# Kernel optimization log

Measured on AMD Instinct MI355X. Metric: run time of the kernel, lower is better.

Reference implementation:

```python
import jax, jax.numpy as jnp
import numpy as np

B, L, S, STATIC = 32, 512, 37, 8
D, DI, N, K, DTR, NL, V = 768, 1536, 16, 4, 48, 4, 32


def _rmsnorm(h, w, eps=1e-5):
    var = jnp.mean(h * h, axis=-1, keepdims=True)
    return h * jax.lax.rsqrt(var + eps) * w


def _layernorm(h, w, b, eps=1e-5):
    mu = jnp.mean(h, axis=-1, keepdims=True)
    var = jnp.mean((h - mu) ** 2, axis=-1, keepdims=True)
    return (h - mu) * jax.lax.rsqrt(var + eps) * w + b


def _selective_scan(u, dt, A, Bm, Cm):
    # u, dt: [B,L,Di]; A: [Di,N]; Bm, Cm: [B,L,N]
    def step(h, inp):
        u_t, dt_t, B_t, C_t = inp              # [B,Di],[B,Di],[B,N],[B,N]
        dA = jnp.exp(dt_t[..., None] * A)      # [B,Di,N]
        h = dA * h + (dt_t * u_t)[..., None] * B_t[:, None, :]
        y = jnp.einsum('bdn,bn->bd', h, C_t)
        return h, y
    h0 = jnp.zeros((u.shape[0], DI, N), u.dtype)
    xs = (u.transpose(1, 0, 2), dt.transpose(1, 0, 2),
          Bm.transpose(1, 0, 2), Cm.transpose(1, 0, 2))
    _, ys = jax.lax.scan(step, h0, xs)
    return ys.transpose(1, 0, 2)  # [B,L,Di]


def setup_inputs() -> dict:
    key = jax.random.key(0)
    ks = jax.random.split(key, 24)
    s = 0.02
    inp = {
        'x': jax.random.normal(ks[0], (B, L, S), jnp.float32),
        'static': jax.random.normal(ks[1], (B, STATIC), jnp.float32),
        'time': jax.random.uniform(ks[2], (B, L), jnp.float32),
        'sensor_mask': jax.random.randint(ks[3], (B, L, S), 0, 2, jnp.int32),
        'labels': jax.random.randint(ks[4], (B, L), 0, V, jnp.int64),
        # CEHR embedding params
        'emb_w': jax.random.normal(ks[5], (D, 2 * S), jnp.float32) * s,
        'emb_b': jnp.zeros((D,), jnp.float32),
        'static_w': jax.random.normal(ks[6], (D, STATIC), jnp.float32) * s,
        'static_b': jnp.zeros((D,), jnp.float32),
        'ln_w': jnp.ones((D,), jnp.float32),
        'ln_b': jnp.zeros((D,), jnp.float32),
        # Mamba layers (stacked)
        'norm_w': jnp.ones((NL, D), jnp.float32),
        'in_proj_w': jax.random.normal(ks[7], (NL, 2 * DI, D), jnp.float32) * s,
        'conv_w': jax.random.normal(ks[8], (NL, DI, K), jnp.float32) * s,
        'conv_b': jnp.zeros((NL, DI), jnp.float32),
        'x_proj_w': jax.random.normal(ks[9], (NL, DTR + 2 * N, DI), jnp.float32) * s,
        'dt_proj_w': jax.random.normal(ks[10], (NL, DI, DTR), jnp.float32) * s,
        'dt_proj_b': jnp.full((NL, DI), -4.6, jnp.float32),  # softplus^-1(~0.01)
        'A_log': jnp.broadcast_to(jnp.log(jnp.arange(1, N + 1, dtype=jnp.float32)), (NL, DI, N)).copy(),
        'D_param': jnp.ones((NL, DI), jnp.float32),
        'out_proj_w': jax.random.normal(ks[11], (NL, D, DI), jnp.float32) * s,
        'norm_f_w': jnp.ones((D,), jnp.float32),
        'lm_head_w': jax.random.normal(ks[12], (V, D), jnp.float32) * s,
    }
    return inp


def reference(x, static, time, sensor_mask, labels, emb_w, emb_b, static_w,
              static_b, ln_w, ln_b, norm_w, in_proj_w, conv_w, conv_b,
              x_proj_w, dt_proj_w, dt_proj_b, A_log, D_param, out_proj_w,
              norm_f_w, lm_head_w):
    # ---- CEHR embedding: concat(values, mask) -> D, plus static broadcast ----
    feats = jnp.concatenate([x, sensor_mask.astype(x.dtype)], axis=-1)  # [B,L,2S]
    h = jnp.einsum('blf,df->bld', feats, emb_w) + emb_b
    h = h + (static @ static_w.T + static_b)[:, None, :]
    h = _layernorm(h, ln_w, ln_b)  # [B,L,D]

    # ---- Mamba backbone ----
    for l in range(NL):
        resid = h
        hn = _rmsnorm(h, norm_w[l])
        xz = jnp.einsum('bld,ed->ble', hn, in_proj_w[l])  # [B,L,2*Di]
        xb, z = jnp.split(xz, 2, axis=-1)
        # causal depthwise conv1d, kernel K
        xp = jnp.pad(xb, ((0, 0), (K - 1, 0), (0, 0)))
        xc = sum(conv_w[l][:, k] * xp[:, k:k + L, :] for k in range(K)) + conv_b[l]
        xc = jax.nn.silu(xc)
        proj = jnp.einsum('bld,ed->ble', xc, x_proj_w[l])  # [B,L,DTR+2N]
        dt_r = proj[..., :DTR]
        Bm = proj[..., DTR:DTR + N]
        Cm = proj[..., DTR + N:]
        dt = jax.nn.softplus(jnp.einsum('blr,dr->bld', dt_r, dt_proj_w[l]) + dt_proj_b[l])
        A = -jnp.exp(A_log[l])  # [Di,N]
        y = _selective_scan(xc, dt, A, Bm, Cm) + D_param[l] * xc
        y = y * jax.nn.silu(z)
        h = resid + jnp.einsum('ble,de->bld', y, out_proj_w[l])

    h = _rmsnorm(h, norm_f_w)
    logits = jnp.einsum('bld,vd->blv', h, lm_head_w)  # [B,L,V]
    return logits
```

## Files before the change

### kernel.cpp

```cpp
#include <hip/hip_runtime.h>
#include <math.h>

#define B_ 32
#define L_ 512
#define S_ 37
#define STATIC_ 8
#define D_ 768
#define DI_ 1536
#define N_ 16
#define DTR_ 48
#define NL_ 4
#define V_ 32
#define ROWS_ (B_*L_)
#define CB_ 8
#define CROWS_ (CB_*L_)
#define NCH_ (B_/CB_)
#define KE_ 96
#define TCH_ 64
#define NCHT_ (L_/TCH_)
#define TP4_ 68
#define KS_ 4
#define KSL_ (DI_/KS_)

typedef __bf16 bf16;
typedef __bf16 bf16x8 __attribute__((ext_vector_type(8)));
typedef __bf16 bf16x4 __attribute__((ext_vector_type(4)));
typedef __bf16 bf16x2 __attribute__((ext_vector_type(2)));
typedef float f32x4 __attribute__((ext_vector_type(4)));

typedef __attribute__((address_space(3))) void lds_void;
typedef __attribute__((address_space(1))) const void gmem_void;

__device__ __forceinline__ void gld16(const void* g, void* l) {
    __builtin_amdgcn_global_load_lds((gmem_void*)g, (lds_void*)l, 16, 0, 0);
}

__device__ __forceinline__ float silu_(float x) { return x / (1.f + __expf(-x)); }
__device__ __forceinline__ float softplus_(float x) {
    return fmaxf(x, 0.f) + __logf(1.f + __expf(-fabsf(x)));
}
__device__ __forceinline__ unsigned pack_bf2_(float a, float b) {
    bf16x2 v{(bf16)a, (bf16)b};
    return __builtin_bit_cast(unsigned, v);
}
template<int CTRL>
__device__ __forceinline__ float dpp_add_(float p) {
    int vi = __builtin_amdgcn_update_dpp(0, __builtin_bit_cast(int, p),
                                         CTRL, 0xF, 0xF, true);
    return p + __builtin_bit_cast(float, vi);
}

template<int MODE>
__global__ __launch_bounds__(256) void gemm_mfma(
    const bf16* __restrict__ A, const bf16* __restrict__ W,
    const float* __restrict__ addsrc, void* __restrict__ Cv,
    int Nstore, int K, int ntn,
    const float* __restrict__ dt_bias, unsigned* __restrict__ swg,
    float* __restrict__ pbuf, const bf16* __restrict__ uref)
{
    __shared__ bf16 As[128 * 32];
    __shared__ bf16 Bs[128 * 32];
    const int tid = threadIdx.x;

    int m0, n0, kbeg, kend;
    if (MODE == 4) {
        m0 = blockIdx.y * 128; n0 = 0;
        kbeg = blockIdx.x * KSL_; kend = kbeg + KSL_;
    } else {
        int bid = blockIdx.x;
        int xcd = bid & 7, slot = bid >> 3;
        int Mtiles = gridDim.x / ntn;
        int mband = Mtiles >> 3;
        int m_tile = xcd * mband + slot / ntn;
        int n_tile = slot % ntn;
        m0 = m_tile * 128; n0 = n_tile * 128;
        kbeg = 0; kend = K;
    }

    f32x4 acc[4][4];
    #pragma unroll
    for (int i = 0; i < 4; i++)
        #pragma unroll
        for (int j = 0; j < 4; j++)
            acc[i][j] = f32x4{0.f, 0.f, 0.f, 0.f};

    const int srow = tid >> 2, spart = tid & 3;
    const bf16* ag = A + (size_t)(m0 + srow) * K + spart * 8;
    const bf16* wg = W + (size_t)(n0 + srow) * K + spart * 8;
    char* lA = (char*)As + tid * 16;
    char* lB = (char*)Bs + tid * 16;

    const int lane = tid & 63, wv = tid >> 6;
    const int wr = wv >> 1, wc = wv & 1;
    const int colL = lane & 15, quad = lane >> 4;
    const bf16* aRd = As + (wr * 64 + colL) * 32 + quad * 8;
    const bf16* bRd = Bs + (wc * 64 + colL) * 32 + quad * 8;

    for (int kt = kbeg; kt < kend; kt += 32) {
        gld16(ag + kt, lA);
        gld16(ag + kt + (size_t)64 * K, lA + 4096);
        gld16(wg + kt, lB);
        gld16(wg + kt + (size_t)64 * K, lB + 4096);
        __syncthreads();
        bf16x8 fa[4], fb[4];
        #pragma unroll
        for (int i = 0; i < 4; i++) fa[i] = *(const bf16x8*)(aRd + i * 16 * 32);
        #pragma unroll
        for (int j = 0; j < 4; j++) fb[j] = *(const bf16x8*)(bRd + j * 16 * 32);
        #pragma unroll
        for (int i = 0; i < 4; i++)
            #pragma unroll
            for (int j = 0; j < 4; j++)
                acc[i][j] = __builtin_amdgcn_mfma_f32_16x16x32_bf16(fa[i], fb[j], acc[i][j], 0, 0, 0);
        __syncthreads();
    }

    float* Cf = (float*)Cv;
    bf16*  Cb = (bf16*)Cv;
    #pragma unroll
    for (int i = 0; i < 4; i++) {
        #pragma unroll
        for (int j = 0; j < 4; j++) {
            int n = n0 + wc * 64 + j * 16 + colL;
            #pragma unroll
            for (int r = 0; r < 4; r++) {
                int m = m0 + wr * 64 + i * 16 + quad * 4 + r;
                float v = acc[i][j][r];
                if (MODE == 2) {
                    float dtv = softplus_(v + dt_bias[n]);
                    float u = (float)uref[(size_t)m * DI_ + n];
                    swg[(size_t)m * DI_ + n] = pack_bf2_(dtv * u, dtv);
                } else if (MODE == 4) {
                    if (n < 96)
                        pbuf[((size_t)blockIdx.x * CROWS_ + m) * 96 + n] = v;
                } else if (n < Nstore) {
                    if (addsrc) v += addsrc[(size_t)m * Nstore + n];
                    if (MODE == 1) Cb[(size_t)m * Nstore + n] = (bf16)v;
                    else           Cf[(size_t)m * Nstore + n] = v;
                }
            }
        }
    }
}

template<int MODE>
__global__ __launch_bounds__(512, 2) void gemm256(
    const bf16* __restrict__ A, const bf16* __restrict__ W,
    const float* __restrict__ addsrc, void* __restrict__ Cv,
    int Nstore, int K, int ntn)
{
    __shared__ bf16 lds[65536];
    const int tid = threadIdx.x;

    const int bid = blockIdx.x;
    const int qx = gridDim.x >> 3;
    const int wgid = (bid & 7) * qx + (bid >> 3);
    const int m0 = (wgid / ntn) * 256;
    const int n0 = (wgid % ntn) * 256;

    const int r0 = tid >> 3;
    const int scol = ((tid & 7) * 8) ^ ((r0 & 7) << 3);
    const size_t sK = (size_t)K;
    const bf16* aSrc = A + (size_t)(m0 + r0) * sK + scol;
    const bf16* bSrc = W + (size_t)(n0 + r0) * sK + scol;
    char* ldst = (char*)lds + tid * 16;

#define STAGE_A(h, t) { const bf16* s_ = aSrc + (size_t)(h) * 128 * sK + (t) * 64;   \
    char* d_ = ldst + ((t) & 1) * 65536 + (h) * 16384;                               \
    gld16(s_, d_); gld16(s_ + 64 * sK, d_ + 8192); }
#define STAGE_B(h, t) { const bf16* s_ = bSrc + (size_t)(h) * 128 * sK + (t) * 64;   \
    char* d_ = ldst + ((t) & 1) * 65536 + 32768 + (h) * 16384;                       \
    gld16(s_, d_); gld16(s_ + 64 * sK, d_ + 8192); }

    const int lane = tid & 63, w = tid >> 6;
    const int wr = w >> 2, wc = w & 3;
    const int colL = lane & 15, quad = lane >> 4;
    const int sx = (colL & 7) << 3;
    const int c0 = (quad * 8) ^ sx;
    const int c1 = c0 ^ 32;
    const bf16* aRd0 = lds + wr * 8192 + colL * 64 + c0;
    const bf16* aRd1 = lds + wr * 8192 + colL * 64 + c1;
    const bf16* bRd0 = lds + 16384 + (wc >> 1) * 8192 + ((wc & 1) * 64 + colL) * 64 + c0;
    const bf16* bRd1 = lds + 16384 + (wc >> 1) * 8192 + ((wc & 1) * 64 + colL) * 64 + c1;

    f32x4 acc[8][4];
    #pragma unroll
    for (int i = 0; i < 8; i++)
        #pragma unroll
        for (int j = 0; j < 4; j++)
            acc[i][j] = f32x4{0.f, 0.f, 0.f, 0.f};
    bf16x8 aF[4][2], bF[4][2];

#define RD_A(buf, mp) { _Pragma("unroll") for (int i = 0; i < 4; i++) {              \
    aF[i][0] = *(const bf16x8*)(aRd0 + (buf) * 32768 + (mp) * 4096 + i * 1024);      \
    aF[i][1] = *(const bf16x8*)(aRd1 + (buf) * 32768 + (mp) * 4096 + i * 1024); } }
#define RD_B01(buf) { _Pragma("unroll") for (int j = 0; j < 2; j++) {                \
    bF[j][0] = *(const bf16x8*)(bRd0 + (buf) * 32768 + j * 1024);                    \
    bF[j][1] = *(const bf16x8*)(bRd1 + (buf) * 32768 + j * 1024); } }
#define RD_B23(buf) { _Pragma("unroll") for (int j = 0; j < 2; j++) {                \
    bF[2 + j][0] = *(const bf16x8*)(bRd0 + (buf) * 32768 + (2 + j) * 1024);          \
    bF[2 + j][1] = *(const bf16x8*)(bRd1 + (buf) * 32768 + (2 + j) * 1024); } }
#define MM(mp, np) { _Pragma("unroll") for (int i = 0; i < 4; i++)                   \
    _Pragma("unroll") for (int j = 0; j < 2; j++) {                                  \
    acc[(mp)*4+i][(np)*2+j] = __builtin_amdgcn_mfma_f32_16x16x32_bf16(               \
        aF[i][0], bF[(np)*2+j][0], acc[(mp)*4+i][(np)*2+j], 0, 0, 0);                \
    acc[(mp)*4+i][(np)*2+j] = __builtin_amdgcn_mfma_f32_16x16x32_bf16(               \
        aF[i][1], bF[(np)*2+j][1], acc[(mp)*4+i][(np)*2+j], 0, 0, 0); } }
#define MID_SYNC  __builtin_amdgcn_s_barrier();                                      \
    asm volatile("s_waitcnt lgkmcnt(0)" ::: "memory");                               \
    __builtin_amdgcn_sched_barrier(0);                                               \
    __builtin_amdgcn_s_setprio(1);
#define END_PHASE __builtin_amdgcn_s_setprio(0); __builtin_amdgcn_s_barrier();

    const int NT = K >> 6;
    const int NI = NT >> 1;

    STAGE_B(0, 0); STAGE_B(1, 0); STAGE_A(0, 0); STAGE_A(1, 0);
    STAGE_B(0, 1); STAGE_B(1, 1);
    asm volatile("s_waitcnt vmcnt(4)" ::: "memory");
    __builtin_amdgcn_s_barrier();

    for (int it = 0; it < NI; ++it) {
        const int t0 = 2 * it, t1 = t0 + 1;
        const bool nlast = (it + 1 < NI);
        RD_A(0, 0); RD_B01(0);
        STAGE_A(0, t1);
        MID_SYNC; MM(0, 0); END_PHASE;
        RD_B23(0);
        STAGE_A(1, t1);
        MID_SYNC; MM(0, 1); END_PHASE;
        RD_A(0, 1);
        if (nlast) STAGE_B(0, t0 + 2);
        MID_SYNC; MM(1, 0); END_PHASE;
        if (nlast) STAGE_B(1, t0 + 2);
        MID_SYNC; MM(1, 1);
        __builtin_amdgcn_s_setprio(0);
        if (nlast) { asm volatile("s_waitcnt vmcnt(4)" ::: "memory"); }
        else       { asm volatile("s_waitcnt vmcnt(0)" ::: "memory"); }
        __builtin_amdgcn_s_barrier();
        RD_A(1, 0); RD_B01(1);
        if (nlast) STAGE_A(0, t0 + 2);
        MID_SYNC; MM(0, 0); END_PHASE;
        RD_B23(1);
        if (nlast) STAGE_A(1, t0 + 2);
        MID_SYNC; MM(0, 1); END_PHASE;
        RD_A(1, 1);
        if (nlast) STAGE_B(0, t1 + 2);
        MID_SYNC; MM(1, 0); END_PHASE;
        if (nlast) STAGE_B(1, t1 + 2);
        MID_SYNC; MM(1, 1);
        __builtin_amdgcn_s_setprio(0);
        if (nlast) { asm volatile("s_waitcnt vmcnt(4)" ::: "memory"); }
        __builtin_amdgcn_s_barrier();
    }

    float* Cf = (float*)Cv;
    bf16*  Cb = (bf16*)Cv;
    #pragma unroll
    for (int f = 0; f < 8; f++) {
        #pragma unroll
        for (int j = 0; j < 4; j++) {
            int n = n0 + wc * 64 + j * 16 + colL;
            #pragma unroll
            for (int r = 0; r < 4; r++) {
                int m = m0 + wr * 128 + f * 16 + quad * 4 + r;
                float v = acc[f][j][r];
                if (MODE == 0) {
                    v += addsrc[(size_t)m * Nstore + n];
                    Cf[(size_t)m * Nstore + n] = v;
                } else {
                    Cb[(size_t)m * Nstore + n] = (bf16)v;
                }
            }
        }
    }
#undef STAGE_A
#undef STAGE_B
#undef RD_A
#undef RD_B01
#undef RD_B23
#undef MM
#undef MID_SYNC
#undef END_PHASE
}

__global__ __launch_bounds__(256) void xpost_kernel(const float* __restrict__ pbuf,
                                                    bf16* __restrict__ dtr,
                                                    bf16* __restrict__ bcb) {
    int idx = blockIdx.x * 256 + threadIdx.x;
    int m = idx / 96, j = idx % 96;
    float s = pbuf[idx];
    #pragma unroll
    for (int k = 1; k < KS_; k++) s += pbuf[(size_t)k * CROWS_ * 96 + idx];
    if (j < 64) {
        dtr[(size_t)m * 64 + j] = (bf16)s;
    } else {
        int jj = j - 64;
        int n = jj & 15, hi = jj >> 4;
        bcb[(size_t)m * 32 + 2 * n + hi] = (bf16)s;
    }
}

__global__ __launch_bounds__(256) void cast_f2b_kernel(const float* __restrict__ s,
                                                       bf16* __restrict__ d) {
    size_t i = (size_t)blockIdx.x * 256 + threadIdx.x;
    d[i] = (bf16)s[i];
}

__global__ __launch_bounds__(256) void pad_lm_kernel(const float* __restrict__ s, bf16* __restrict__ d) {
    int i = blockIdx.x * 256 + threadIdx.x;
    int row = i / D_;
    d[i] = (row < V_) ? (bf16)s[i] : (bf16)0.f;
}

__global__ __launch_bounds__(256) void pad_embw_kernel(const float* __restrict__ s, bf16* __restrict__ d) {
    int i = blockIdx.x * 256 + threadIdx.x;
    int row = i / KE_, col = i % KE_;
    d[i] = (col < 2 * S_) ? (bf16)s[row * 2 * S_ + col] : (bf16)0.f;
}

__global__ __launch_bounds__(256) void feats_kernel(const float* __restrict__ x,
                                                    const int* __restrict__ mask,
                                                    bf16* __restrict__ d) {
    size_t i = (size_t)blockIdx.x * 256 + threadIdx.x;
    size_t row = i / KE_;
    int col = (int)(i % KE_);
    float v = 0.f;
    if (col < S_) v = x[row * S_ + col];
    else if (col < 2 * S_) v = (float)mask[row * S_ + (col - S_)];
    d[i] = (bf16)v;
}

__global__ __launch_bounds__(256) void xpw_pad_kernel(const float* __restrict__ xpw,
                                                      bf16* __restrict__ d) {
    int l = blockIdx.y;
    int idx = blockIdx.x * 256 + threadIdx.x;
    int row = idx / DI_, col = idx % DI_;
    float v = 0.f;
    if (row < DTR_) v = xpw[((size_t)l * (DTR_ + 2 * N_) + row) * DI_ + col];
    else if (row >= 64 && row < 96) v = xpw[((size_t)l * (DTR_ + 2 * N_) + row - 16) * DI_ + col];
    d[(size_t)l * 128 * DI_ + idx] = (bf16)v;
}

__global__ __launch_bounds__(256) void dtw_pad_kernel(const float* __restrict__ dtw,
                                                      bf16* __restrict__ d) {
    int l = blockIdx.y;
    int idx = blockIdx.x * 256 + threadIdx.x;
    int row = idx / 64, c = idx % 64;
    float v = (c < DTR_) ? dtw[((size_t)l * DI_ + row) * DTR_ + c] : 0.f;
    d[(size_t)l * DI_ * 64 + idx] = (bf16)v;
}

__global__ __launch_bounds__(256) void sstat_kernel(const float* __restrict__ stat,
                                                    const float* __restrict__ static_w,
                                                    const float* __restrict__ static_b,
                                                    const float* __restrict__ emb_b,
                                                    float* __restrict__ sstat) {
    int i = blockIdx.x * 256 + threadIdx.x;
    int d = i % D_, b = i / D_;
    float acc = emb_b[d] + static_b[d];
    const float* sw = static_w + (size_t)d * STATIC_;
    const float* sv = stat + (size_t)b * STATIC_;
    #pragma unroll
    for (int s = 0; s < STATIC_; s++) acc += sv[s] * sw[s];
    sstat[i] = acc;
}

__device__ __forceinline__ void block_reduce2_(float& a, float& b, float* sbuf) {
    #pragma unroll
    for (int off = 32; off > 0; off >>= 1) {
        a += __shfl_down(a, off, 64);
        b += __shfl_down(b, off, 64);
    }
    int lane = threadIdx.x & 63, wid = threadIdx.x >> 6;
    if (lane == 0) { sbuf[wid] = a; sbuf[4 + wid] = b; }
    __syncthreads();
    a = sbuf[0] + sbuf[1] + sbuf[2] + sbuf[3];
    b = sbuf[4] + sbuf[5] + sbuf[6] + sbuf[7];
}

__global__ __launch_bounds__(256) void ln_embed_kernel(const float* __restrict__ h_pre,
                                                       const float* __restrict__ sstat,
                                                       const float* __restrict__ ln_w,
                                                       const float* __restrict__ ln_b,
                                                       float* __restrict__ h) {
    int row = blockIdx.x, b = row / L_, tid = threadIdx.x;
    __shared__ float sbuf[8];
    float v[3], sum = 0.f, sq = 0.f;
    #pragma unroll
    for (int j = 0; j < 3; j++) {
        int d = tid + 256 * j;
        v[j] = h_pre[(size_t)row * D_ + d] + sstat[b * D_ + d];
        sum += v[j]; sq += v[j] * v[j];
    }
    block_reduce2_(sum, sq, sbuf);
    float mu = sum * (1.f / D_);
    float rstd = rsqrtf(sq * (1.f / D_) - mu * mu + 1e-5f);
    #pragma unroll
    for (int j = 0; j < 3; j++) {
        int d = tid + 256 * j;
        h[(size_t)row * D_ + d] = (v[j] - mu) * rstd * ln_w[d] + ln_b[d];
    }
}

__global__ __launch_bounds__(256) void rmsnorm_bf_kernel(const float* __restrict__ h,
                                                         const float* __restrict__ w,
                                                         bf16* __restrict__ out) {
    int row = blockIdx.x, tid = threadIdx.x;
    __shared__ float sbuf[8];
    float v[3], ss = 0.f, dummy = 0.f;
    #pragma unroll
    for (int j = 0; j < 3; j++) {
        v[j] = h[(size_t)row * D_ + tid + 256 * j];
        ss += v[j] * v[j];
    }
    block_reduce2_(ss, dummy, sbuf);
    float rstd = rsqrtf(ss * (1.f / D_) + 1e-5f);
    #pragma unroll
    for (int j = 0; j < 3; j++) {
        int d = tid + 256 * j;
        out[(size_t)row * D_ + d] = (bf16)(v[j] * rstd * w[d]);
    }
}

__global__ __launch_bounds__(256) void conv_silu_kernel(const bf16* __restrict__ xzb,
                                                        const float* __restrict__ cw,
                                                        const float* __restrict__ cb,
                                                        const float* __restrict__ Dp,
                                                        bf16* __restrict__ xcb,
                                                        unsigned* __restrict__ gag) {
    size_t idx = (size_t)blockIdx.x * 256 + threadIdx.x;
    int d4 = (int)(idx % (DI_ / 4));
    size_t row = idx / (DI_ / 4);
    int t = (int)(row % L_);
    int d = d4 * 4;
    const uint2* xz64 = (const uint2*)xzb;
    size_t base = row * 768 + d4;
    uint2 z2{0u, 0u};
    uint2 p0  = xz64[base];
    uint2 pm1 = (t >= 1) ? xz64[base - 768]     : z2;
    uint2 pm2 = (t >= 2) ? xz64[base - 2 * 768] : z2;
    uint2 pm3 = (t >= 3) ? xz64[base - 3 * 768] : z2;
    uint2 pz  = xz64[base + 384];

    bf16x4 a0 = __builtin_bit_cast(bf16x4, p0);
    bf16x4 a1 = __builtin_bit_cast(bf16x4, pm1);
    bf16x4 a2 = __builtin_bit_cast(bf16x4, pm2);
    bf16x4 a3 = __builtin_bit_cast(bf16x4, pm3);
    bf16x4 az = __builtin_bit_cast(bf16x4, pz);

    float cbl[4], Dl[4];
    *(float4*)cbl = ((const float4*)cb)[d4];
    *(float4*)Dl  = ((const float4*)Dp)[d4];

    float u[4];
    unsigned gv[4];
    #pragma unroll
    for (int c = 0; c < 4; c++) {
        float4 wc = ((const float4*)cw)[d + c];
        float acc = cbl[c] + wc.x * (float)a3[c] + wc.y * (float)a2[c]
                           + wc.z * (float)a1[c] + wc.w * (float)a0[c];
        u[c] = silu_(acc);
        float gz = silu_((float)az[c]);
        gv[c] = pack_bf2_(Dl[c] * u[c] * gz, gz);
    }
    ((uint2*)xcb)[row * (DI_ / 4) + d4] = uint2{pack_bf2_(u[0], u[1]), pack_bf2_(u[2], u[3])};
    *(uint4*)(gag + row * DI_ + d) = uint4{gv[0], gv[1], gv[2], gv[3]};
}

__global__ __launch_bounds__(256) void scan_lds_kernel(const unsigned* __restrict__ bcp,
                                                       const unsigned* __restrict__ swg,
                                                       const unsigned* __restrict__ gag,
                                                       const float* __restrict__ A_log,
                                                       bf16* __restrict__ yb) {
    __shared__ unsigned lsw[2][16][TP4_];
    __shared__ unsigned lga[2][16][TP4_];
    __shared__ unsigned lbc[2][16][TP4_];
    const int tid = threadIdx.x;
    const int n = tid & 15, dl = tid >> 4;
    const int d = blockIdx.x * 16 + dl;
    const int b = blockIdx.y;
    const float AvL = -__expf(A_log[(size_t)d * N_ + n]) * 1.44269504f;
    const size_t seqbase = (size_t)b * L_;
    const int d0 = blockIdx.x * 16;

    unsigned swr[4], gar[4], bcr[4];

    #define GLOAD(c)                                                        \
        {                                                                   \
            size_t rb = seqbase + (size_t)(c) * TCH_;                       \
            _Pragma("unroll")                                               \
            for (int i = 0; i < 4; i++) {                                   \
                size_t g = rb + i * 16 + dl;                                \
                swr[i] = swg[g * DI_ + d0 + n];                             \
                gar[i] = gag[g * DI_ + d0 + n];                             \
                bcr[i] = bcp[g * 16 + n];                                   \
            }                                                               \
        }
    #define DSWRITE(p)                                                      \
        {                                                                   \
            _Pragma("unroll")                                               \
            for (int i = 0; i < 4; i++) {                                   \
                int t = i * 16 + dl;                                        \
                lsw[p][n][t] = swr[i];                                      \
                lga[p][n][t] = gar[i];                                      \
                lbc[p][n][t] = bcr[i];                                      \
            }                                                               \
        }

    GLOAD(0);
    DSWRITE(0);
    __syncthreads();
    GLOAD(1);

    float h = 0.f;
    for (int c = 0; c < NCHT_; c++) {
        int p = c & 1;
        bf16* py = yb + (seqbase + (size_t)c * TCH_) * DI_ + d;
        #pragma unroll 4
        for (int t0 = 0; t0 < TCH_; t0 += 4) {
            uint4 s4 = *(const uint4*)&lsw[p][dl][t0];
            uint4 b4 = *(const uint4*)&lbc[p][n][t0];
            uint4 g4{0u, 0u, 0u, 0u};
            if (n == 0) g4 = *(const uint4*)&lga[p][dl][t0];
            unsigned ss[4] = {s4.x, s4.y, s4.z, s4.w};
            unsigned bb[4] = {b4.x, b4.y, b4.z, b4.w};
            unsigned gg[4] = {g4.x, g4.y, g4.z, g4.w};
            #pragma unroll
            for (int u = 0; u < 4; u++) {
                bf16x2 dv = __builtin_bit_cast(bf16x2, ss[u]);
                bf16x2 bcv = __builtin_bit_cast(bf16x2, bb[u]);
                float du = (float)dv.x, dtv = (float)dv.y;
                float dA = __builtin_amdgcn_exp2f(dtv * AvL);
                h = dA * h + du * (float)bcv.x;
                float pq = h * (float)bcv.y;
                pq = dpp_add_<0xB1>(pq);
                pq = dpp_add_<0x4E>(pq);
                pq = dpp_add_<0x124>(pq);
                pq = dpp_add_<0x128>(pq);
                if (n == 0) {
                    bf16x2 og = __builtin_bit_cast(bf16x2, gg[u]);
                    py[(size_t)(t0 + u) * DI_] = (bf16)(pq * (float)og.y + (float)og.x);
                }
            }
        }
        if (c + 1 < NCHT_) {
            DSWRITE(p ^ 1);
            __syncthreads();
            if (c + 2 < NCHT_) GLOAD(c + 2);
        }
    }
    #undef GLOAD
    #undef DSWRITE
}

extern "C" void kernel_launch(void* const* d_in, const int* in_sizes, int n_in,
                              void* d_out, int out_size, void* d_ws, size_t ws_size,
                              hipStream_t stream) {
    const float* x        = (const float*)d_in[0];
    const float* stat     = (const float*)d_in[1];
    const int*   mask     = (const int*)d_in[3];
    const float* emb_w    = (const float*)d_in[5];
    const float* emb_b    = (const float*)d_in[6];
    const float* static_w = (const float*)d_in[7];
    const float* static_b = (const float*)d_in[8];
    const float* ln_w     = (const float*)d_in[9];
    const float* ln_b     = (const float*)d_in[10];
    const float* norm_w   = (const float*)d_in[11];
    const float* in_proj_w  = (const float*)d_in[12];
    const float* conv_w   = (const float*)d_in[13];
    const float* conv_b   = (const float*)d_in[14];
    const float* x_proj_w = (const float*)d_in[15];
    const float* dt_proj_w= (const float*)d_in[16];
    const float* dt_proj_b= (const float*)d_in[17];
    const float* A_log    = (const float*)d_in[18];
    const float* D_param  = (const float*)d_in[19];
    const float* out_proj_w = (const float*)d_in[20];
    const float* norm_f_w = (const float*)d_in[21];
    const float* lm_head_w= (const float*)d_in[22];
    float* out = (float*)d_out;

    char* p = (char*)d_ws;
    float*    h      = (float*)p;         p += (size_t)ROWS_ * D_ * 4;
    bf16*     hn_bf  = (bf16*)p;          p += (size_t)CROWS_ * D_ * 2;
    char*     xz_region = p;
    bf16*     xz_bf  = (bf16*)p;          p += (size_t)CROWS_ * 2 * DI_ * 2;
    bf16*     xc_bf  = (bf16*)p;          p += (size_t)CROWS_ * DI_ * 2;
    unsigned* sw_g   = (unsigned*)p;      p += (size_t)CROWS_ * DI_ * 4;
    unsigned* gate_g = (unsigned*)p;      p += (size_t)CROWS_ * DI_ * 4;
    bf16*     bc16   = (bf16*)p;          p += (size_t)CROWS_ * 32 * 2;
    bf16*     dtr_bf = (bf16*)p;          p += (size_t)CROWS_ * 64 * 2;
    float*    pbuf   = (float*)p;         p += (size_t)KS_ * CROWS_ * 96 * 4;
    bf16*     y_bf   = (bf16*)p;          p += (size_t)ROWS_ * DI_ * 2;
    bf16*     inw_l  = (bf16*)p;          p += (size_t)2 * DI_ * D_ * 2;
    bf16*     outw_l = (bf16*)p;          p += (size_t)D_ * DI_ * 2;
    bf16*     xpwp_bf= (bf16*)p;          p += (size_t)NL_ * 128 * DI_ * 2;
    bf16*     dtwp_bf= (bf16*)p;          p += (size_t)NL_ * DI_ * 64 * 2;
    bf16*     lmw_bf = (bf16*)p;          p += (size_t)128 * D_ * 2;
    bf16*     embw_bf= (bf16*)p;          p += (size_t)D_ * KE_ * 2;
    bf16*     feats  = (bf16*)p;          p += (size_t)ROWS_ * KE_ * 2;
    float*    sstat  = (float*)p;         p += (size_t)B_ * D_ * 4;
    float*    h_pre  = (float*)xz_region;
    bf16*     hn_full= (bf16*)sw_g;

    pad_lm_kernel<<<(128 * D_) / 256, 256, 0, stream>>>(lm_head_w, lmw_bf);
    pad_embw_kernel<<<(D_ * KE_) / 256, 256, 0, stream>>>(emb_w, embw_bf);
    feats_kernel<<<(ROWS_ * KE_) / 256, 256, 0, stream>>>(x, mask, feats);
    dim3 gxp((128 * DI_) / 256, NL_);
    xpw_pad_kernel<<<gxp, 256, 0, stream>>>(x_proj_w, xpwp_bf);
    dim3 gdt((DI_ * 64) / 256, NL_);
    dtw_pad_kernel<<<gdt, 256, 0, stream>>>(dt_proj_w, dtwp_bf);
    sstat_kernel<<<(B_ * D_) / 256, 256, 0, stream>>>(stat, static_w, static_b, emb_b, sstat);

    gemm_mfma<0><<<(D_ / 128) * (ROWS_ / 128), 256, 0, stream>>>(
        feats, embw_bf, nullptr, h_pre, D_, KE_, D_ / 128,
        nullptr, nullptr, nullptr, nullptr);
    ln_embed_kernel<<<ROWS_, 256, 0, stream>>>(h_pre, sstat, ln_w, ln_b, h);

    for (int l = 0; l < NL_; l++) {
        cast_f2b_kernel<<<(2 * DI_ * D_) / 256, 256, 0, stream>>>(
            in_proj_w + (size_t)l * 2 * DI_ * D_, inw_l);
        cast_f2b_kernel<<<(D_ * DI_) / 256, 256, 0, stream>>>(
            out_proj_w + (size_t)l * D_ * DI_, outw_l);

        for (int c = 0; c < NCH_; c++) {
            float* hc = h + (size_t)c * CROWS_ * D_;

            rmsnorm_bf_kernel<<<CROWS_, 256, 0, stream>>>(hc, norm_w + (size_t)l * D_, hn_bf);

            gemm256<1><<<(CROWS_ / 256) * (2 * DI_ / 256), 512, 0, stream>>>(
                hn_bf, inw_l, nullptr, xz_bf, 2 * DI_, D_, 2 * DI_ / 256);

            conv_silu_kernel<<<(CROWS_ * DI_ / 4) / 256, 256, 0, stream>>>(
                xz_bf, conv_w + (size_t)l * DI_ * 4, conv_b + (size_t)l * DI_,
                D_param + (size_t)l * DI_, xc_bf, gate_g);

            dim3 g2a(KS_, CROWS_ / 128);
            gemm_mfma<4><<<g2a, 256, 0, stream>>>(xc_bf, xpwp_bf + (size_t)l * 128 * DI_,
                                                  nullptr, nullptr, 0, DI_, 1,
                                                  nullptr, nullptr, pbuf, nullptr);
            xpost_kernel<<<(CROWS_ * 96) / 256, 256, 0, stream>>>(pbuf, dtr_bf, bc16);

            gemm_mfma<2><<<(DI_ / 128) * (CROWS_ / 128), 256, 0, stream>>>(
                dtr_bf, dtwp_bf + (size_t)l * DI_ * 64, nullptr, nullptr, 0, 64, DI_ / 128,
                dt_proj_b + (size_t)l * DI_, sw_g, nullptr, xc_bf);

            dim3 gs(DI_ / 16, CB_);
            scan_lds_kernel<<<gs, 256, 0, stream>>>((const unsigned*)bc16, sw_g, gate_g,
                                                    A_log + (size_t)l * DI_ * N_,
                                                    y_bf + (size_t)c * CROWS_ * DI_);
        }

        gemm256<0><<<(ROWS_ / 256) * (D_ / 256), 512, 0, stream>>>(
            y_bf, outw_l, h, h, D_, DI_, D_ / 256);
    }

    rmsnorm_bf_kernel<<<ROWS_, 256, 0, stream>>>(h, norm_f_w, hn_full);
    gemm_mfma<0><<<ROWS_ / 128, 256, 0, stream>>>(
        hn_full, lmw_bf, nullptr, out, V_, D_, 1,
        nullptr, nullptr, nullptr, nullptr);
}
```

Measured before the change: 2.740 ms.

## Restructure selective scan: fp32 swizzled B/C tiles, async LDS loads, batched output writes

xpost now writes B and C as fp32 into a per-chunk, XOR-swizzled 8KB tile layout. The scan kernel pulls these tiles straight into LDS with global_load_lds and double-buffers them. The scan kernel also stores dt/u pre-converted to float2 in LDS, which removes per-step bf16 conversions. The output is collected across 16 timesteps so that each lane writes one y value, replacing writes made only by lane n==0. This reduces ALU and store divergence in the scan inner loop, at the cost of doubling the B/C buffer size and using more LDS.

Measured after the change: 2.403 ms. 1.14x faster.

```diff
diff --git a/kernel.cpp b/kernel.cpp
--- a/kernel.cpp
+++ b/kernel.cpp
@@ -18,9 +18,10 @@
 #define KE_ 96
 #define TCH_ 64
 #define NCHT_ (L_/TCH_)
-#define TP4_ 68
 #define KS_ 4
 #define KSL_ (DI_/KS_)
+#define TPW_ 66
+#define TPO_ 68
 
 typedef __bf16 bf16;
 typedef __bf16 bf16x8 __attribute__((ext_vector_type(8)));
@@ -286,7 +287,7 @@
 
 __global__ __launch_bounds__(256) void xpost_kernel(const float* __restrict__ pbuf,
                                                     bf16* __restrict__ dtr,
-                                                    bf16* __restrict__ bcb) {
+                                                    float* __restrict__ bcf) {
     int idx = blockIdx.x * 256 + threadIdx.x;
     int m = idx / 96, j = idx % 96;
     float s = pbuf[idx];
@@ -297,7 +298,10 @@
     } else {
         int jj = j - 64;
         int n = jj & 15, hi = jj >> 4;
-        bcb[(size_t)m * 32 + 2 * n + hi] = (bf16)s;
+        int bb = m >> 9, t = m & 511;
+        int ct = t >> 6, tl = t & 63;
+        int byo = (n * 512 + tl * 8 + hi * 4) ^ ((n & 7) << 4);
+        *(float*)((char*)bcf + (size_t)(bb * 8 + ct) * 8192 + byo) = s;
     }
 }
 
@@ -468,89 +472,86 @@
     *(uint4*)(gag + row * DI_ + d) = uint4{gv[0], gv[1], gv[2], gv[3]};
 }
 
-__global__ __launch_bounds__(256) void scan_lds_kernel(const unsigned* __restrict__ bcp,
+__global__ __launch_bounds__(256) void scan_lds_kernel(const float* __restrict__ bcf,
                                                        const unsigned* __restrict__ swg,
                                                        const unsigned* __restrict__ gag,
                                                        const float* __restrict__ A_log,
                                                        bf16* __restrict__ yb) {
-    __shared__ unsigned lsw[2][16][TP4_];
-    __shared__ unsigned lga[2][16][TP4_];
-    __shared__ unsigned lbc[2][16][TP4_];
+    __shared__ float2   lsw2[2][16][TPW_];
+    __shared__ char     lbcf[2][8192];
+    __shared__ unsigned logds[2][16][TPO_];
     const int tid = threadIdx.x;
     const int n = tid & 15, dl = tid >> 4;
-    const int d = blockIdx.x * 16 + dl;
+    const int d0 = blockIdx.x * 16;
+    const int d = d0 + dl;
     const int b = blockIdx.y;
     const float AvL = -__expf(A_log[(size_t)d * N_ + n]) * 1.44269504f;
     const size_t seqbase = (size_t)b * L_;
-    const int d0 = blockIdx.x * 16;
-
-    unsigned swr[4], gar[4], bcr[4];
-
-    #define GLOAD(c)                                                        \
-        {                                                                   \
-            size_t rb = seqbase + (size_t)(c) * TCH_;                       \
-            _Pragma("unroll")                                               \
-            for (int i = 0; i < 4; i++) {                                   \
-                size_t g = rb + i * 16 + dl;                                \
-                swr[i] = swg[g * DI_ + d0 + n];                             \
-                gar[i] = gag[g * DI_ + d0 + n];                             \
-                bcr[i] = bcp[g * 16 + n];                                   \
-            }                                                               \
-        }
-    #define DSWRITE(p)                                                      \
-        {                                                                   \
-            _Pragma("unroll")                                               \
-            for (int i = 0; i < 4; i++) {                                   \
-                int t = i * 16 + dl;                                        \
-                lsw[p][n][t] = swr[i];                                      \
-                lga[p][n][t] = gar[i];                                      \
-                lbc[p][n][t] = bcr[i];                                      \
-            }                                                               \
-        }
-
-    GLOAD(0);
+
+    const char* bcf_base = (const char*)bcf + (size_t)b * NCHT_ * 8192;
+    unsigned swr[4], gar[4];
+
+    #define BCF_GLD(c) { const char* s_ = bcf_base + (size_t)(c) * 8192 + tid * 16;  \
+        char* d_ = (char*)lbcf + ((c) & 1) * 8192 + tid * 16;                        \
+        gld16(s_, d_); gld16(s_ + 4096, d_ + 4096); }
+    #define REG_LOAD(c) { size_t rb = seqbase + (size_t)(c) * TCH_;                  \
+        _Pragma("unroll") for (int i = 0; i < 4; i++) {                              \
+            size_t g = (rb + dl + 16 * i) * DI_ + d0 + n;                            \
+            swr[i] = swg[g]; gar[i] = gag[g]; } }
+    #define DSWRITE(p) { _Pragma("unroll") for (int i = 0; i < 4; i++) {             \
+            int t = dl + 16 * i;                                                     \
+            bf16x2 w2 = __builtin_bit_cast(bf16x2, swr[i]);                          \
+            lsw2[p][n][t] = float2{(float)w2.x, (float)w2.y};                        \
+            logds[p][n][t] = gar[i]; } }
+
+    BCF_GLD(0);
+    REG_LOAD(0);
     DSWRITE(0);
     __syncthreads();
-    GLOAD(1);
+    REG_LOAD(1);
 
     float h = 0.f;
     for (int c = 0; c < NCHT_; c++) {
-        int p = c & 1;
-        bf16* py = yb + (seqbase + (size_t)c * TCH_) * DI_ + d;
-        #pragma unroll 4
-        for (int t0 = 0; t0 < TCH_; t0 += 4) {
-            uint4 s4 = *(const uint4*)&lsw[p][dl][t0];
-            uint4 b4 = *(const uint4*)&lbc[p][n][t0];
-            uint4 g4{0u, 0u, 0u, 0u};
-            if (n == 0) g4 = *(const uint4*)&lga[p][dl][t0];
-            unsigned ss[4] = {s4.x, s4.y, s4.z, s4.w};
-            unsigned bb[4] = {b4.x, b4.y, b4.z, b4.w};
-            unsigned gg[4] = {g4.x, g4.y, g4.z, g4.w};
+        const int p = c & 1;
+        if (c + 1 < NCHT_) BCF_GLD(c + 1);
+        bf16* pyc = yb + (seqbase + (size_t)c * TCH_) * DI_ + d;
+        const char* bcrow = (const char*)lbcf + p * 8192;
+        #pragma unroll
+        for (int tb = 0; tb < TCH_; tb += 16) {
+            float res = 0.f;
             #pragma unroll
-            for (int u = 0; u < 4; u++) {
-                bf16x2 dv = __builtin_bit_cast(bf16x2, ss[u]);
-                bf16x2 bcv = __builtin_bit_cast(bf16x2, bb[u]);
-                float du = (float)dv.x, dtv = (float)dv.y;
-                float dA = __builtin_amdgcn_exp2f(dtv * AvL);
-                h = dA * h + du * (float)bcv.x;
-                float pq = h * (float)bcv.y;
-                pq = dpp_add_<0xB1>(pq);
-                pq = dpp_add_<0x4E>(pq);
-                pq = dpp_add_<0x124>(pq);
-                pq = dpp_add_<0x128>(pq);
-                if (n == 0) {
-                    bf16x2 og = __builtin_bit_cast(bf16x2, gg[u]);
-                    py[(size_t)(t0 + u) * DI_] = (bf16)(pq * (float)og.y + (float)og.x);
+            for (int tq = 0; tq < 16; tq += 2) {
+                float4 dd = *(const float4*)&lsw2[p][dl][tb + tq];
+                int byo = (n * 512 + (tb + tq) * 8) ^ ((n & 7) << 4);
+                float4 bc = *(const float4*)(bcrow + byo);
+                #pragma unroll
+                for (int u = 0; u < 2; u++) {
+                    float du  = u ? dd.z : dd.x;
+                    float dtv = u ? dd.w : dd.y;
+                    float Bv  = u ? bc.z : bc.x;
+                    float Cv  = u ? bc.w : bc.y;
+                    float dA = __builtin_amdgcn_exp2f(dtv * AvL);
+                    h = dA * h + du * Bv;
+                    float pq = h * Cv;
+                    pq = dpp_add_<0xB1>(pq);
+                    pq = dpp_add_<0x4E>(pq);
+                    pq = dpp_add_<0x124>(pq);
+                    pq = dpp_add_<0x128>(pq);
+                    if (n == tq + u) res = pq;
                 }
             }
+            unsigned og = logds[p][dl][tb + n];
+            bf16x2 o2 = __builtin_bit_cast(bf16x2, og);
+            pyc[(size_t)(tb + n) * DI_] = (bf16)(res * (float)o2.y + (float)o2.x);
         }
         if (c + 1 < NCHT_) {
             DSWRITE(p ^ 1);
             __syncthreads();
-            if (c + 2 < NCHT_) GLOAD(c + 2);
+            if (c + 2 < NCHT_) REG_LOAD(c + 2);
         }
     }
-    #undef GLOAD
+    #undef BCF_GLD
+    #undef REG_LOAD
     #undef DSWRITE
 }
 
@@ -588,7 +589,7 @@
     bf16*     xc_bf  = (bf16*)p;          p += (size_t)CROWS_ * DI_ * 2;
     unsigned* sw_g   = (unsigned*)p;      p += (size_t)CROWS_ * DI_ * 4;
     unsigned* gate_g = (unsigned*)p;      p += (size_t)CROWS_ * DI_ * 4;
-    bf16*     bc16   = (bf16*)p;          p += (size_t)CROWS_ * 32 * 2;
+    float*    bcf    = (float*)p;         p += (size_t)CROWS_ * 32 * 4;
     bf16*     dtr_bf = (bf16*)p;          p += (size_t)CROWS_ * 64 * 2;
     float*    pbuf   = (float*)p;         p += (size_t)KS_ * CROWS_ * 96 * 4;
     bf16*     y_bf   = (bf16*)p;          p += (size_t)ROWS_ * DI_ * 2;
@@ -639,14 +640,14 @@
             gemm_mfma<4><<<g2a, 256, 0, stream>>>(xc_bf, xpwp_bf + (size_t)l * 128 * DI_,
                                                   nullptr, nullptr, 0, DI_, 1,
                                                   nullptr, nullptr, pbuf, nullptr);
-            xpost_kernel<<<(CROWS_ * 96) / 256, 256, 0, stream>>>(pbuf, dtr_bf, bc16);
+            xpost_kernel<<<(CROWS_ * 96) / 256, 256, 0, stream>>>(pbuf, dtr_bf, bcf);
 
             gemm_mfma<2><<<(DI_ / 128) * (CROWS_ / 128), 256, 0, stream>>>(
                 dtr_bf, dtwp_bf + (size_t)l * DI_ * 64, nullptr, nullptr, 0, 64, DI_ / 128,
                 dt_proj_b + (size_t)l * DI_, sw_g, nullptr, xc_bf);
 
             dim3 gs(DI_ / 16, CB_);
-            scan_lds_kernel<<<gs, 256, 0, stream>>>((const unsigned*)bc16, sw_g, gate_g,
+            scan_lds_kernel<<<gs, 256, 0, stream>>>(bcf, sw_g, gate_g,
                                                     A_log + (size_t)l * DI_ * N_,
                                                     y_bf + (size_t)c * CROWS_ * DI_);
         }
```
